# Kernel tuning notes

Hardware: AMD Instinct MI355X
Metric: run time of the kernel (lower is better)

Reference implementation:

```python
import jax, jax.numpy as jnp
import numpy as np

N_NODES = 50000
N_EDGES = 1600000
IN_DIM = 128
OUT_DIM = 128
PRELU_INIT = 0.25
EPS = 1e-8


def setup_inputs() -> dict:
    key = jax.random.key(0)
    k_seq, k_w, k_r, k_c = jax.random.split(key, 4)
    seq = jax.random.normal(k_seq, (N_NODES, IN_DIM), dtype=jnp.float32)
    # xavier_normal_ with gain=1.414 on a [out_dim, in_dim] Linear weight
    std = 1.414 * np.sqrt(2.0 / (IN_DIM + OUT_DIM))
    W = jax.random.normal(k_w, (OUT_DIM, IN_DIM), dtype=jnp.float32) * std
    alpha = jnp.full((1,), PRELU_INIT, dtype=jnp.float32)
    rows = jax.random.randint(k_r, (N_EDGES,), 0, N_NODES)  # destination node per edge
    cols = jax.random.randint(k_c, (N_EDGES,), 0, N_NODES)  # source node per edge
    return {"seq": seq, "W": W, "alpha": alpha, "rows": rows, "cols": cols}


def reference(seq, W, alpha, rows, cols):
    # fc: seq @ W.T  -> [N, out_dim]
    seq_fts = seq @ W.T
    # spmm(adj, seq_fts): sum features of source nodes into destination rows
    agg = jax.ops.segment_sum(seq_fts[cols], rows, num_segments=N_NODES)
    # spmm(adj, ones): per-row degree
    deg = jax.ops.segment_sum(jnp.ones((rows.shape[0],), dtype=seq.dtype), rows,
                              num_segments=N_NODES)
    out = agg / (deg[:, None] + EPS)
    # PReLU with single shared parameter alpha
    return jnp.where(out >= 0, out, alpha[0] * out)
```

## Files before the change

### kernel.cpp

```cpp
#include <hip/hip_runtime.h>

#define N_NODES 50000
#define N_EDGES 1600000
#define DIM 128
#define NPB 32
#define NB 1563
#define SEG_CAP 1408
#define EPB 4096
#define NBLK 391
#define EPT (EPB / 512)
#define HPS 1568
#define QSCALE 22.0f
#define QINV (1.0f / 22.0f)


typedef __attribute__((ext_vector_type(8))) short bf16x8;
typedef __attribute__((ext_vector_type(4))) float f32x4;

__device__ __forceinline__ unsigned short f2bf_rne(float f) {
    unsigned b = __float_as_uint(f);
    return (unsigned short)((b + 0x7FFFu + ((b >> 16) & 1u)) >> 16);
}

__device__ __forceinline__ unsigned q4(float4 v) {
    int a = __float2int_rn(v.x * QSCALE);
    int b = __float2int_rn(v.y * QSCALE);
    int c = __float2int_rn(v.z * QSCALE);
    int d = __float2int_rn(v.w * QSCALE);
    return (unsigned)(a & 255) | ((unsigned)(b & 255) << 8) |
           ((unsigned)(c & 255) << 16) | ((unsigned)(d & 255) << 24);
}

__global__ __launch_bounds__(512) void p1_k(const int* __restrict__ rows,
                                            const int* __restrict__ cols,
                                            unsigned* __restrict__ packed,
                                            unsigned short* __restrict__ hp,
                                            const float* __restrict__ seq,
                                            unsigned* __restrict__ seq8,
                                            const float* __restrict__ W,
                                            unsigned short* __restrict__ W16) {
    __shared__ int lh[NB];
    __shared__ int lcur[NB];
    __shared__ unsigned stg[EPB];
    __shared__ int wtot[8];
    int t = threadIdx.x, blk = blockIdx.x;
    for (int i = t; i < NB; i += 512) lh[i] = 0;
    __syncthreads();
    int base = blk * EPB;
    int er[EPT], ec[EPT];
#pragma unroll
    for (int it = 0; it < EPT; ++it) {
        int e = base + it * 512 + t;
        if (e < N_EDGES) {
            er[it] = rows[e];
            ec[it] = cols[e];
            atomicAdd(&lh[er[it] >> 5], 1);
        } else {
            er[it] = -1;
            ec[it] = 0;
        }
    }
    const float4* s4 = (const float4*)seq;
    for (int i = blk * 512 + t; i < N_NODES * DIM / 4; i += NBLK * 512)
        seq8[i] = q4(s4[i]);
    if (blk == 0) {
        const float4* w4 = (const float4*)W;
        ushort4* o4 = (ushort4*)W16;
        for (int i = t; i < DIM * DIM / 4; i += 512) {
            float4 v = w4[i];
            ushort4 o;
            o.x = f2bf_rne(v.x);
            o.y = f2bf_rne(v.y);
            o.z = f2bf_rne(v.z);
            o.w = f2bf_rne(v.w);
            o4[i] = o;
        }
    }
    __syncthreads();
    int myb = 4 * t;
    int c0 = 0, c1 = 0, c2 = 0, c3 = 0, s = 0;
    if (myb < NB) {
        c0 = lh[myb];
        c1 = (myb + 1 < NB) ? lh[myb + 1] : 0;
        c2 = (myb + 2 < NB) ? lh[myb + 2] : 0;
        c3 = (myb + 3 < NB) ? lh[myb + 3] : 0;
        s = c0 + c1 + c2 + c3;
    }
    int x = s;
#pragma unroll
    for (int o = 1; o < 64; o <<= 1) {
        int u = __shfl_up(x, o);
        if ((t & 63) >= o) x += u;
    }
    if ((t & 63) == 63) wtot[t >> 6] = x;
    __syncthreads();
    int off = 0;
    for (int ww = 0; ww < (t >> 6); ++ww) off += wtot[ww];
    if (myb < NB) {
        int r = off + x - s;
        unsigned short* hrow = hp + blk * HPS;
        lcur[myb] = r; r += c0; hrow[myb] = (unsigned short)r;
        if (myb + 1 < NB) { lcur[myb + 1] = r; r += c1; hrow[myb + 1] = (unsigned short)r; }
        if (myb + 2 < NB) { lcur[myb + 2] = r; r += c2; hrow[myb + 2] = (unsigned short)r; }
        if (myb + 3 < NB) { lcur[myb + 3] = r; r += c3; hrow[myb + 3] = (unsigned short)r; }
    }
    __syncthreads();
#pragma unroll
    for (int it = 0; it < EPT; ++it) {
        int r = er[it];
        if (r >= 0) {
            int pos = atomicAdd(&lcur[r >> 5], 1);
            stg[pos] = ((unsigned)(r & 31) << 16) | (unsigned)ec[it];
        }
    }
    __syncthreads();
    const uint4* sv = (const uint4*)stg;
    uint4* dv = (uint4*)(packed + blk * EPB);
    for (int i = t; i < EPB / 4; i += 512) dv[i] = sv[i];
}

__global__ __launch_bounds__(256) void prep_k(const unsigned* __restrict__ packed,
                                              const unsigned short* __restrict__ hp,
                                              unsigned short* __restrict__ colsg,
                                              int* __restrict__ histg) {
    __shared__ unsigned rawl[SEG_CAP];
    __shared__ int srcidx[SEG_CAP];
    __shared__ unsigned short colsl[SEG_CAP];
    __shared__ int hist[NPB];
    __shared__ int lcur[NPB];
    __shared__ int wsum[4];
    __shared__ int rawn;
    int b = blockIdx.x, t = threadIdx.x;
    if (t < NPB) hist[t] = 0;

    int cnt0 = 0, st0 = 0, cnt1 = 0, st1 = 0;
    if (t < NBLK) {
        const unsigned short* hr = hp + t * HPS;
        int e = hr[b];
        st0 = b ? hr[b - 1] : 0;
        cnt0 = e - st0;
    }
    if (t + 256 < NBLK) {
        const unsigned short* hr = hp + (t + 256) * HPS;
        int e = hr[b];
        st1 = b ? hr[b - 1] : 0;
        cnt1 = e - st1;
    }
    int cnt = cnt0 + cnt1;
    int x = cnt;
#pragma unroll
    for (int o = 1; o < 64; o <<= 1) {
        int u = __shfl_up(x, o);
        if ((t & 63) >= o) x += u;
    }
    if ((t & 63) == 63) wsum[t >> 6] = x;
    __syncthreads();
    int off = 0;
    for (int ww = 0; ww < (t >> 6); ++ww) off += wsum[ww];
    int rp = off + x - cnt;
    if (t == 255) rawn = off + x;
    if (cnt > 0 && rp + cnt <= SEG_CAP) {
        int s0 = t * EPB + st0;
        for (int k = 0; k < cnt0; ++k) srcidx[rp + k] = s0 + k;
        int s1 = (t + 256) * EPB + st1;
        for (int k = 0; k < cnt1; ++k) srcidx[rp + cnt0 + k] = s1 + k;
    }
    __syncthreads();
    int n = min(rawn, SEG_CAP);
    for (int i = t; i < n; i += 256) {
        unsigned p = packed[srcidx[i]];
        rawl[i] = p;
        atomicAdd(&hist[p >> 16], 1);
    }
    __syncthreads();
    if (t < NPB) {
        int v = hist[t], xx = v;
#pragma unroll
        for (int o = 1; o < 32; o <<= 1) {
            int u = __shfl_up(xx, o);
            if (t >= o) xx += u;
        }
        lcur[t] = xx - v;
    }
    __syncthreads();
    for (int i = t; i < n; i += 256) {
        unsigned p = rawl[i];
        int pos = atomicAdd(&lcur[p >> 16], 1);
        colsl[pos] = (unsigned short)(p & 0xFFFFu);
    }
    __syncthreads();
    int n2 = (n + 1) >> 1;
    const unsigned* cv = (const unsigned*)colsl;
    unsigned* dst = (unsigned*)(colsg + b * SEG_CAP);
    for (int i = t; i < n2; i += 256) dst[i] = cv[i];
    if (t < NPB) histg[b * NPB + t] = hist[t];
}

#define ACC4(u)                                 \
    {                                           \
        s0 += (int)(signed char)((u) & 0xFF);   \
        s1 += (int)(signed char)(((u) >> 8) & 0xFF); \
        s2 += (int)(signed char)(((u) >> 16) & 0xFF); \
        s3 += ((int)(u)) >> 24;                 \
    }

__global__ __launch_bounds__(256) void aggemm_k(const unsigned* __restrict__ seqQ,
                                                const unsigned short* __restrict__ colsg,
                                                const int* __restrict__ histg,
                                                const unsigned short* __restrict__ W16,
                                                const float* __restrict__ alpha_p,
                                                float* __restrict__ out) {
    __shared__ unsigned short colsl[SEG_CAP];
    __shared__ unsigned meanL[NPB * 68];
    __shared__ int histl[NPB];
    __shared__ int lbase[NPB];
    int b = blockIdx.x, t = threadIdx.x;
    if (t < NPB) {
        int v = histg[b * NPB + t];
        histl[t] = v;
        int xx = v;
#pragma unroll
        for (int o = 1; o < 32; o <<= 1) {
            int u = __shfl_up(xx, o);
            if (t >= o) xx += u;
        }
        lbase[t] = xx - v;
    }
    __syncthreads();
    int n = lbase[NPB - 1] + histl[NPB - 1];
    int n2 = (n + 1) >> 1;
    const unsigned* src = (const unsigned*)(colsg + b * SEG_CAP);
    unsigned* cd = (unsigned*)colsl;
    for (int i = t; i < n2; i += 256) cd[i] = src[i];
    __syncthreads();

    int w = t >> 6, lane = t & 63;
    int h = lane >> 5, l = lane & 31;
#pragma unroll 1
    for (int ii = 0; ii < 8; ++ii) {
        int ln = w * 8 + ii;
        int node = b * NPB + ln;
        int base = lbase[ln], d = histl[ln];
        int s0 = 0, s1 = 0, s2 = 0, s3 = 0;
        if (node < N_NODES) {
            int j = 0;
            for (; j + 32 <= d; j += 32) {
                unsigned cc[16];
#pragma unroll
                for (int q = 0; q < 16; ++q) cc[q] = colsl[base + j + 2 * q + h];
                unsigned uu[16];
#pragma unroll
                for (int q = 0; q < 16; ++q) uu[q] = seqQ[cc[q] * 32 + l];
#pragma unroll
                for (int q = 0; q < 16; ++q) ACC4(uu[q])
            }
            if (j + 16 <= d) {
                unsigned cc[8];
#pragma unroll
                for (int q = 0; q < 8; ++q) cc[q] = colsl[base + j + 2 * q + h];
                unsigned uu[8];
#pragma unroll
                for (int q = 0; q < 8; ++q) uu[q] = seqQ[cc[q] * 32 + l];
#pragma unroll
                for (int q = 0; q < 8; ++q) ACC4(uu[q])
                j += 16;
            }
            if (j + 8 <= d) {
                unsigned c0 = colsl[base + j + h];
                unsigned c1 = colsl[base + j + 2 + h];
                unsigned c2 = colsl[base + j + 4 + h];
                unsigned c3 = colsl[base + j + 6 + h];
                unsigned u0 = seqQ[c0 * 32 + l];
                unsigned u1 = seqQ[c1 * 32 + l];
                unsigned u2 = seqQ[c2 * 32 + l];
                unsigned u3 = seqQ[c3 * 32 + l];
                ACC4(u0) ACC4(u1) ACC4(u2) ACC4(u3)
                j += 8;
            }
            for (; j < d; j += 2) {
                int e = j + h;
                if (e < d) {
                    unsigned u = seqQ[colsl[base + e] * 32 + l];
                    ACC4(u)
                }
            }
        }
        s0 += __shfl_xor(s0, 32);
        s1 += __shfl_xor(s1, 32);
        s2 += __shfl_xor(s2, 32);
        s3 += __shfl_xor(s3, 32);
        float inv = QINV / ((float)d + 1e-8f);
        int sa = h ? s2 : s0;
        int sb = h ? s3 : s1;
        unsigned rx = (unsigned)f2bf_rne((float)sa * inv);
        unsigned ry = (unsigned)f2bf_rne((float)sb * inv);
        meanL[ln * 68 + 2 * l + h] = (node < N_NODES) ? (rx | (ry << 16)) : 0u;
    }
    __syncthreads();

    int lane15 = lane & 15, quad = lane >> 4;
    bf16x8 bfr[2][4];
#pragma unroll
    for (int cg = 0; cg < 2; ++cg) {
        int col = (w + 4 * cg) * 16 + lane15;
#pragma unroll
        for (int kc = 0; kc < 4; ++kc)
            bfr[cg][kc] = *(const bf16x8*)(W16 + col * 128 + kc * 32 + quad * 8);
    }
    float al = alpha_p[0];
    const unsigned short* mbase = (const unsigned short*)meanL;

#pragma unroll
    for (int m = 0; m < 2; ++m) {
        bf16x8 afr[4];
#pragma unroll
        for (int kc = 0; kc < 4; ++kc)
            afr[kc] = *(const bf16x8*)(mbase + (m * 16 + lane15) * 136 + kc * 32 + quad * 8);
        int row0 = b * NPB + m * 16 + quad * 4;
#pragma unroll
        for (int cg = 0; cg < 2; ++cg) {
            f32x4 acc = {0.f, 0.f, 0.f, 0.f};
#pragma unroll
            for (int kc = 0; kc < 4; ++kc)
                acc = __builtin_amdgcn_mfma_f32_16x16x32_bf16(afr[kc], bfr[cg][kc], acc, 0, 0, 0);
#pragma unroll
            for (int r = 0; r < 4; ++r) {
                int row = row0 + r;
                if (row < N_NODES) {
                    float v = acc[r];
                    v = v >= 0.f ? v : al * v;
                    out[row * DIM + (w + 4 * cg) * 16 + lane15] = v;
                }
            }
        }
    }
}

extern "C" void kernel_launch(void* const* d_in, const int* in_sizes, int n_in,
                              void* d_out, int out_size, void* d_ws, size_t ws_size,
                              hipStream_t stream) {
    const float* seq = (const float*)d_in[0];
    const float* W = (const float*)d_in[1];
    const float* alpha = (const float*)d_in[2];
    const int* rows = (const int*)d_in[3];
    const int* cols = (const int*)d_in[4];
    float* out = (float*)d_out;

    char* ws = (char*)d_ws;
    unsigned* seq8 = (unsigned*)(ws);
    unsigned short* W16 = (unsigned short*)(ws + 6400000);
    unsigned* packed = (unsigned*)(ws + 6432768);
    unsigned short* hp = (unsigned short*)(ws + 12838912);
    unsigned short* colsg = (unsigned short*)(ws + 14065088);
    int* histg = (int*)(ws + 18466496);

    p1_k<<<NBLK, 512, 0, stream>>>(rows, cols, packed, hp, seq, seq8, W, W16);
    prep_k<<<NB, 256, 0, stream>>>(packed, hp, colsg, histg);
    aggemm_k<<<NB, 256, 0, stream>>>(seq8, colsg, histg, W16, alpha, out);
}
```

Before: 157.1 us.

## Split quantized features into two half-dimension arrays and gather in two passes

The int8-quantized node feature table is split into a low half (dims 0-63) and a high half (dims 64-127), each stored as a separate 3.2 MB array. The aggregation gathers each half in its own pass, with 16 lanes per row and 4 edges in flight per wavefront. The aim is a smaller working set per pass that fits better in L2/MALL, giving more gather hits. The cost is reading the column lists twice and more shuffle reductions per node.

```diff
diff --git a/kernel.cpp b/kernel.cpp
--- a/kernel.cpp
+++ b/kernel.cpp
@@ -36,7 +36,8 @@
                                             unsigned* __restrict__ packed,
                                             unsigned short* __restrict__ hp,
                                             const float* __restrict__ seq,
-                                            unsigned* __restrict__ seq8,
+                                            unsigned* __restrict__ seq8lo,
+                                            unsigned* __restrict__ seq8hi,
                                             const float* __restrict__ W,
                                             unsigned short* __restrict__ W16) {
     __shared__ int lh[NB];
@@ -61,8 +62,12 @@
         }
     }
     const float4* s4 = (const float4*)seq;
-    for (int i = blk * 512 + t; i < N_NODES * DIM / 4; i += NBLK * 512)
-        seq8[i] = q4(s4[i]);
+    for (int i = blk * 512 + t; i < N_NODES * DIM / 4; i += NBLK * 512) {
+        unsigned v = q4(s4[i]);
+        int node = i >> 5, dq = i & 31;
+        unsigned* dst = (dq < 16) ? seq8lo : seq8hi;
+        dst[node * 16 + (dq & 15)] = v;
+    }
     if (blk == 0) {
         const float4* w4 = (const float4*)W;
         ushort4* o4 = (ushort4*)W16;
@@ -204,7 +209,8 @@
         s3 += ((int)(u)) >> 24;                 \
     }
 
-__global__ __launch_bounds__(256) void aggemm_k(const unsigned* __restrict__ seqQ,
+__global__ __launch_bounds__(256) void aggemm_k(const unsigned* __restrict__ seqLo,
+                                                const unsigned* __restrict__ seqHi,
                                                 const unsigned short* __restrict__ colsg,
                                                 const int* __restrict__ histg,
                                                 const unsigned short* __restrict__ W16,
@@ -235,66 +241,61 @@
     __syncthreads();
 
     int w = t >> 6, lane = t & 63;
-    int h = lane >> 5, l = lane & 31;
+    int e4 = lane >> 4, l16 = lane & 15;
 #pragma unroll 1
-    for (int ii = 0; ii < 8; ++ii) {
-        int ln = w * 8 + ii;
-        int node = b * NPB + ln;
-        int base = lbase[ln], d = histl[ln];
-        int s0 = 0, s1 = 0, s2 = 0, s3 = 0;
-        if (node < N_NODES) {
-            int j = 0;
-            for (; j + 32 <= d; j += 32) {
-                unsigned cc[16];
-#pragma unroll
-                for (int q = 0; q < 16; ++q) cc[q] = colsl[base + j + 2 * q + h];
-                unsigned uu[16];
-#pragma unroll
-                for (int q = 0; q < 16; ++q) uu[q] = seqQ[cc[q] * 32 + l];
-#pragma unroll
-                for (int q = 0; q < 16; ++q) ACC4(uu[q])
-            }
-            if (j + 16 <= d) {
-                unsigned cc[8];
-#pragma unroll
-                for (int q = 0; q < 8; ++q) cc[q] = colsl[base + j + 2 * q + h];
-                unsigned uu[8];
-#pragma unroll
-                for (int q = 0; q < 8; ++q) uu[q] = seqQ[cc[q] * 32 + l];
-#pragma unroll
-                for (int q = 0; q < 8; ++q) ACC4(uu[q])
-                j += 16;
-            }
-            if (j + 8 <= d) {
-                unsigned c0 = colsl[base + j + h];
-                unsigned c1 = colsl[base + j + 2 + h];
-                unsigned c2 = colsl[base + j + 4 + h];
-                unsigned c3 = colsl[base + j + 6 + h];
-                unsigned u0 = seqQ[c0 * 32 + l];
-                unsigned u1 = seqQ[c1 * 32 + l];
-                unsigned u2 = seqQ[c2 * 32 + l];
-                unsigned u3 = seqQ[c3 * 32 + l];
-                ACC4(u0) ACC4(u1) ACC4(u2) ACC4(u3)
-                j += 8;
-            }
-            for (; j < d; j += 2) {
-                int e = j + h;
-                if (e < d) {
-                    unsigned u = seqQ[colsl[base + e] * 32 + l];
-                    ACC4(u)
+    for (int H = 0; H < 2; ++H) {
+        const unsigned* seqH = H ? seqHi : seqLo;
+#pragma unroll 1
+        for (int ii = 0; ii < 8; ++ii) {
+            int ln = w * 8 + ii;
+            int node = b * NPB + ln;
+            int base = lbase[ln], d = histl[ln];
+            int s0 = 0, s1 = 0, s2 = 0, s3 = 0;
+            if (node < N_NODES) {
+                int j = 0;
+                for (; j + 32 <= d; j += 32) {
+                    unsigned cc[8];
+#pragma unroll
+                    for (int q = 0; q < 8; ++q) cc[q] = colsl[base + j + 4 * q + e4];
+                    unsigned uu[8];
+#pragma unroll
+                    for (int q = 0; q < 8; ++q) uu[q] = seqH[cc[q] * 16 + l16];
+#pragma unroll
+                    for (int q = 0; q < 8; ++q) ACC4(uu[q])
+                }
+                if (j + 16 <= d) {
+                    unsigned cc[4];
+#pragma unroll
+                    for (int q = 0; q < 4; ++q) cc[q] = colsl[base + j + 4 * q + e4];
+                    unsigned uu[4];
+#pragma unroll
+                    for (int q = 0; q < 4; ++q) uu[q] = seqH[cc[q] * 16 + l16];
+#pragma unroll
+                    for (int q = 0; q < 4; ++q) ACC4(uu[q])
+                    j += 16;
+                }
+                for (; j < d; j += 4) {
+                    int e = j + e4;
+                    if (e < d) {
+                        unsigned u = seqH[colsl[base + e] * 16 + l16];
+                        ACC4(u)
+                    }
                 }
             }
-        }
-        s0 += __shfl_xor(s0, 32);
-        s1 += __shfl_xor(s1, 32);
-        s2 += __shfl_xor(s2, 32);
-        s3 += __shfl_xor(s3, 32);
-        float inv = QINV / ((float)d + 1e-8f);
-        int sa = h ? s2 : s0;
-        int sb = h ? s3 : s1;
-        unsigned rx = (unsigned)f2bf_rne((float)sa * inv);
-        unsigned ry = (unsigned)f2bf_rne((float)sb * inv);
-        meanL[ln * 68 + 2 * l + h] = (node < N_NODES) ? (rx | (ry << 16)) : 0u;
+            s0 += __shfl_xor(s0, 16); s0 += __shfl_xor(s0, 32);
+            s1 += __shfl_xor(s1, 16); s1 += __shfl_xor(s1, 32);
+            s2 += __shfl_xor(s2, 16); s2 += __shfl_xor(s2, 32);
+            s3 += __shfl_xor(s3, 16); s3 += __shfl_xor(s3, 32);
+            if (e4 < 2) {
+                float inv = QINV / ((float)d + 1e-8f);
+                float va = (e4 ? (float)s2 : (float)s0) * inv;
+                float vb = (e4 ? (float)s3 : (float)s1) * inv;
+                unsigned rx = (unsigned)f2bf_rne(va);
+                unsigned ry = (unsigned)f2bf_rne(vb);
+                meanL[ln * 68 + (H << 5) + 2 * l16 + e4] =
+                    (node < N_NODES) ? (rx | (ry << 16)) : 0u;
+            }
+        }
     }
     __syncthreads();
 
@@ -347,14 +348,15 @@
     float* out = (float*)d_out;
 
     char* ws = (char*)d_ws;
-    unsigned* seq8 = (unsigned*)(ws);
+    unsigned* seq8lo = (unsigned*)(ws);
+    unsigned* seq8hi = (unsigned*)(ws + 3200000);
     unsigned short* W16 = (unsigned short*)(ws + 6400000);
     unsigned* packed = (unsigned*)(ws + 6432768);
     unsigned short* hp = (unsigned short*)(ws + 12838912);
     unsigned short* colsg = (unsigned short*)(ws + 14065088);
     int* histg = (int*)(ws + 18466496);
 
-    p1_k<<<NBLK, 512, 0, stream>>>(rows, cols, packed, hp, seq, seq8, W, W16);
+    p1_k<<<NBLK, 512, 0, stream>>>(rows, cols, packed, hp, seq, seq8lo, seq8hi, W, W16);
     prep_k<<<NB, 256, 0, stream>>>(packed, hp, colsg, histg);
-    aggemm_k<<<NB, 256, 0, stream>>>(seq8, colsg, histg, W16, alpha, out);
-}
+    aggemm_k<<<NB, 256, 0, stream>>>(seq8lo, seq8hi, colsg, histg, W16, alpha, out);
+}
```

After: 176.1 us. +12.1%, slower.

## Batch eight node-blocks per prep block and gather int8 rows with 16-byte loads

Applied to the files above, without the earlier changes.

The prep kernel now handles 8 destination blocks per workgroup: it builds a 256-bin histogram over 8-bit local row ids and scatters columns straight to global memory, with no shared staging. The goal is fewer launches of tiny blocks and less redundant reading of the header table. The aggregation loop now has 8 lanes each load a uint4 (16 int8 features), so 8 edges are handled per wavefront step. This is followed by a three-level shuffle reduction over 16 accumulators. In exchange, register pressure rises, the reduction needs more shuffles, and global scatter writes are uncoalesced.

```diff
diff --git a/kernel.cpp b/kernel.cpp
--- a/kernel.cpp
+++ b/kernel.cpp
@@ -10,6 +10,9 @@
 #define NBLK 391
 #define EPT (EPB / 512)
 #define HPS 1568
+#define BPS 8
+#define PB 196
+#define SCAP8 9472
 #define QSCALE 22.0f
 #define QINV (1.0f / 22.0f)
 
@@ -110,7 +113,7 @@
         int r = er[it];
         if (r >= 0) {
             int pos = atomicAdd(&lcur[r >> 5], 1);
-            stg[pos] = ((unsigned)(r & 31) << 16) | (unsigned)ec[it];
+            stg[pos] = ((unsigned)(r & 255) << 16) | (unsigned)ec[it];
         }
     }
     __syncthreads();
@@ -119,34 +122,27 @@
     for (int i = t; i < EPB / 4; i += 512) dv[i] = sv[i];
 }
 
-__global__ __launch_bounds__(256) void prep_k(const unsigned* __restrict__ packed,
+__global__ __launch_bounds__(512) void prep_k(const unsigned* __restrict__ packed,
                                               const unsigned short* __restrict__ hp,
                                               unsigned short* __restrict__ colsg,
                                               int* __restrict__ histg) {
-    __shared__ unsigned rawl[SEG_CAP];
-    __shared__ int srcidx[SEG_CAP];
-    __shared__ unsigned short colsl[SEG_CAP];
-    __shared__ int hist[NPB];
-    __shared__ int lcur[NPB];
-    __shared__ int wsum[4];
+    __shared__ int srcidx[SCAP8];
+    __shared__ int hist[256];
+    __shared__ int lcur[256];
+    __shared__ int bbase[BPS];
+    __shared__ int wsum[8];
     __shared__ int rawn;
-    int b = blockIdx.x, t = threadIdx.x;
-    if (t < NPB) hist[t] = 0;
-
-    int cnt0 = 0, st0 = 0, cnt1 = 0, st1 = 0;
+    int sb = blockIdx.x, t = threadIdx.x;
+    int b0 = sb * BPS;
+    int bend = min(b0 + BPS, NB) - 1;
+    for (int i = t; i < 256; i += 512) hist[i] = 0;
+    int cnt = 0, st = 0;
     if (t < NBLK) {
         const unsigned short* hr = hp + t * HPS;
-        int e = hr[b];
-        st0 = b ? hr[b - 1] : 0;
-        cnt0 = e - st0;
-    }
-    if (t + 256 < NBLK) {
-        const unsigned short* hr = hp + (t + 256) * HPS;
-        int e = hr[b];
-        st1 = b ? hr[b - 1] : 0;
-        cnt1 = e - st1;
-    }
-    int cnt = cnt0 + cnt1;
+        int e = hr[bend];
+        st = b0 ? hr[b0 - 1] : 0;
+        cnt = e - st;
+    }
     int x = cnt;
 #pragma unroll
     for (int o = 1; o < 64; o <<= 1) {
@@ -158,53 +154,62 @@
     int off = 0;
     for (int ww = 0; ww < (t >> 6); ++ww) off += wsum[ww];
     int rp = off + x - cnt;
-    if (t == 255) rawn = off + x;
-    if (cnt > 0 && rp + cnt <= SEG_CAP) {
-        int s0 = t * EPB + st0;
-        for (int k = 0; k < cnt0; ++k) srcidx[rp + k] = s0 + k;
-        int s1 = (t + 256) * EPB + st1;
-        for (int k = 0; k < cnt1; ++k) srcidx[rp + cnt0 + k] = s1 + k;
-    }
-    __syncthreads();
-    int n = min(rawn, SEG_CAP);
-    for (int i = t; i < n; i += 256) {
+    if (t == 511) rawn = off + x;
+    if (cnt > 0) {
+        if (rp + cnt > SCAP8) cnt = max(0, SCAP8 - rp);
+        int s0 = t * EPB + st;
+        for (int k = 0; k < cnt; ++k) srcidx[rp + k] = s0 + k;
+    }
+    __syncthreads();
+    int n = min(rawn, SCAP8);
+    for (int i = t; i < n; i += 512) {
         unsigned p = packed[srcidx[i]];
-        rawl[i] = p;
-        atomicAdd(&hist[p >> 16], 1);
-    }
-    __syncthreads();
-    if (t < NPB) {
-        int v = hist[t], xx = v;
-#pragma unroll
-        for (int o = 1; o < 32; o <<= 1) {
+        atomicAdd(&hist[(p >> 16) & 255], 1);
+    }
+    __syncthreads();
+    int xx = 0, v = 0;
+    if (t < 256) {
+        v = hist[t];
+        xx = v;
+#pragma unroll
+        for (int o = 1; o < 64; o <<= 1) {
             int u = __shfl_up(xx, o);
-            if (t >= o) xx += u;
-        }
-        lcur[t] = xx - v;
-    }
-    __syncthreads();
-    for (int i = t; i < n; i += 256) {
-        unsigned p = rawl[i];
-        int pos = atomicAdd(&lcur[p >> 16], 1);
-        colsl[pos] = (unsigned short)(p & 0xFFFFu);
-    }
-    __syncthreads();
-    int n2 = (n + 1) >> 1;
-    const unsigned* cv = (const unsigned*)colsl;
-    unsigned* dst = (unsigned*)(colsg + b * SEG_CAP);
-    for (int i = t; i < n2; i += 256) dst[i] = cv[i];
-    if (t < NPB) histg[b * NPB + t] = hist[t];
-}
-
-#define ACC4(u)                                 \
-    {                                           \
-        s0 += (int)(signed char)((u) & 0xFF);   \
-        s1 += (int)(signed char)(((u) >> 8) & 0xFF); \
-        s2 += (int)(signed char)(((u) >> 16) & 0xFF); \
-        s3 += ((int)(u)) >> 24;                 \
-    }
-
-__global__ __launch_bounds__(256) void aggemm_k(const unsigned* __restrict__ seqQ,
+            if ((t & 63) >= o) xx += u;
+        }
+        if ((t & 63) == 63) wsum[t >> 6] = xx;
+    }
+    __syncthreads();
+    if (t < 256) {
+        int off2 = 0;
+        for (int ww = 0; ww < (t >> 6); ++ww) off2 += wsum[ww];
+        int bb = off2 + xx - v;
+        lcur[t] = bb;
+        if ((t & 31) == 0) bbase[t >> 5] = bb;
+    }
+    __syncthreads();
+    for (int i = t; i < n; i += 512) {
+        unsigned p = packed[srcidx[i]];
+        int bin = (p >> 16) & 255;
+        int pos = atomicAdd(&lcur[bin], 1);
+        int k = bin >> 5;
+        int local = pos - bbase[k];
+        if (local < SEG_CAP && b0 + k < NB)
+            colsg[(b0 + k) * SEG_CAP + local] = (unsigned short)(p & 0xFFFFu);
+    }
+    if (t < 256 && b0 + (t >> 5) < NB)
+        histg[(b0 + (t >> 5)) * 32 + (t & 31)] = hist[t];
+}
+
+#define ACCW(vv, o)                                      \
+    {                                                    \
+        s[o] += (int)(signed char)((vv) & 0xFF);         \
+        s[o + 1] += (int)(signed char)(((vv) >> 8) & 0xFF);  \
+        s[o + 2] += (int)(signed char)(((vv) >> 16) & 0xFF); \
+        s[o + 3] += ((int)(vv)) >> 24;                   \
+    }
+#define ACCU(u) { ACCW((u).x, 0) ACCW((u).y, 4) ACCW((u).z, 8) ACCW((u).w, 12) }
+
+__global__ __launch_bounds__(256) void aggemm_k(const uint4* __restrict__ seqV,
                                                 const unsigned short* __restrict__ colsg,
                                                 const int* __restrict__ histg,
                                                 const unsigned short* __restrict__ W16,
@@ -235,66 +240,65 @@
     __syncthreads();
 
     int w = t >> 6, lane = t & 63;
-    int h = lane >> 5, l = lane & 31;
+    int eg = lane >> 3, l4 = lane & 7;
 #pragma unroll 1
     for (int ii = 0; ii < 8; ++ii) {
         int ln = w * 8 + ii;
         int node = b * NPB + ln;
         int base = lbase[ln], d = histl[ln];
-        int s0 = 0, s1 = 0, s2 = 0, s3 = 0;
+        int s[16];
+#pragma unroll
+        for (int m = 0; m < 16; ++m) s[m] = 0;
         if (node < N_NODES) {
             int j = 0;
             for (; j + 32 <= d; j += 32) {
-                unsigned cc[16];
-#pragma unroll
-                for (int q = 0; q < 16; ++q) cc[q] = colsl[base + j + 2 * q + h];
-                unsigned uu[16];
-#pragma unroll
-                for (int q = 0; q < 16; ++q) uu[q] = seqQ[cc[q] * 32 + l];
-#pragma unroll
-                for (int q = 0; q < 16; ++q) ACC4(uu[q])
+                int c0 = colsl[base + j + eg];
+                int c1 = colsl[base + j + 8 + eg];
+                int c2 = colsl[base + j + 16 + eg];
+                int c3 = colsl[base + j + 24 + eg];
+                uint4 u0 = seqV[c0 * 8 + l4];
+                uint4 u1 = seqV[c1 * 8 + l4];
+                uint4 u2 = seqV[c2 * 8 + l4];
+                uint4 u3 = seqV[c3 * 8 + l4];
+                ACCU(u0) ACCU(u1) ACCU(u2) ACCU(u3)
             }
             if (j + 16 <= d) {
-                unsigned cc[8];
-#pragma unroll
-                for (int q = 0; q < 8; ++q) cc[q] = colsl[base + j + 2 * q + h];
-                unsigned uu[8];
-#pragma unroll
-                for (int q = 0; q < 8; ++q) uu[q] = seqQ[cc[q] * 32 + l];
-#pragma unroll
-                for (int q = 0; q < 8; ++q) ACC4(uu[q])
+                int c0 = colsl[base + j + eg];
+                int c1 = colsl[base + j + 8 + eg];
+                uint4 u0 = seqV[c0 * 8 + l4];
+                uint4 u1 = seqV[c1 * 8 + l4];
+                ACCU(u0) ACCU(u1)
                 j += 16;
             }
             if (j + 8 <= d) {
-                unsigned c0 = colsl[base + j + h];
-                unsigned c1 = colsl[base + j + 2 + h];
-                unsigned c2 = colsl[base + j + 4 + h];
-                unsigned c3 = colsl[base + j + 6 + h];
-                unsigned u0 = seqQ[c0 * 32 + l];
-                unsigned u1 = seqQ[c1 * 32 + l];
-                unsigned u2 = seqQ[c2 * 32 + l];
-                unsigned u3 = seqQ[c3 * 32 + l];
-                ACC4(u0) ACC4(u1) ACC4(u2) ACC4(u3)
+                int c0 = colsl[base + j + eg];
+                uint4 u0 = seqV[c0 * 8 + l4];
+                ACCU(u0)
                 j += 8;
             }
-            for (; j < d; j += 2) {
-                int e = j + h;
+            {
+                int e = j + eg;
                 if (e < d) {
-                    unsigned u = seqQ[colsl[base + e] * 32 + l];
-                    ACC4(u)
+                    uint4 u = seqV[colsl[base + e] * 8 + l4];
+                    ACCU(u)
                 }
             }
         }
-        s0 += __shfl_xor(s0, 32);
-        s1 += __shfl_xor(s1, 32);
-        s2 += __shfl_xor(s2, 32);
-        s3 += __shfl_xor(s3, 32);
-        float inv = QINV / ((float)d + 1e-8f);
-        int sa = h ? s2 : s0;
-        int sb = h ? s3 : s1;
-        unsigned rx = (unsigned)f2bf_rne((float)sa * inv);
-        unsigned ry = (unsigned)f2bf_rne((float)sb * inv);
-        meanL[ln * 68 + 2 * l + h] = (node < N_NODES) ? (rx | (ry << 16)) : 0u;
+#pragma unroll
+        for (int m = 0; m < 16; ++m) {
+            s[m] += __shfl_xor(s[m], 8);
+            s[m] += __shfl_xor(s[m], 16);
+            s[m] += __shfl_xor(s[m], 32);
+        }
+        if (eg == 0) {
+            float inv = QINV / ((float)d + 1e-8f);
+#pragma unroll
+            for (int m = 0; m < 8; ++m) {
+                unsigned rx = (unsigned)f2bf_rne((float)s[2 * m] * inv);
+                unsigned ry = (unsigned)f2bf_rne((float)s[2 * m + 1] * inv);
+                meanL[ln * 68 + l4 * 8 + m] = (node < N_NODES) ? (rx | (ry << 16)) : 0u;
+            }
+        }
     }
     __syncthreads();
 
@@ -355,6 +359,6 @@
     int* histg = (int*)(ws + 18466496);
 
     p1_k<<<NBLK, 512, 0, stream>>>(rows, cols, packed, hp, seq, seq8, W, W16);
-    prep_k<<<NB, 256, 0, stream>>>(packed, hp, colsg, histg);
-    aggemm_k<<<NB, 256, 0, stream>>>(seq8, colsg, histg, W16, alpha, out);
-}
+    prep_k<<<PB, 512, 0, stream>>>(packed, hp, colsg, histg);
+    aggemm_k<<<NB, 256, 0, stream>>>((const uint4*)seq8, colsg, histg, W16, alpha, out);
+}
```

New measurement: 169.6 us. 7.9% more time.
